# Optimization experiments

Hardware: AMD Instinct MI355X
Metric: run time of the kernel (lower is better)

Reference implementation:

```python
import jax, jax.numpy as jnp
import numpy as np

V = 32000   # vocab_size
H = 256     # num_hiddens
B = 32      # batch
T = 128     # seq_len


def setup_inputs() -> dict:
    key = jax.random.key(0)
    ks = jax.random.split(key, 10)
    s = 0.05  # keep pre-activations in a sane range
    return {
        "X": jax.random.randint(ks[0], (B, T), 0, V),
        "H0": jnp.zeros((B, H), jnp.float32),
        "Wz": (jax.random.normal(ks[1], (H, V + H)) * s).astype(jnp.float32),
        "bz": (jax.random.normal(ks[2], (H,)) * s).astype(jnp.float32),
        "Wr": (jax.random.normal(ks[3], (H, V + H)) * s).astype(jnp.float32),
        "br": (jax.random.normal(ks[4], (H,)) * s).astype(jnp.float32),
        "Wh": (jax.random.normal(ks[5], (H, V + H)) * s).astype(jnp.float32),
        "bh": (jax.random.normal(ks[6], (H,)) * s).astype(jnp.float32),
        "Wo": (jax.random.normal(ks[7], (V, H)) * s).astype(jnp.float32),
        "bo": (jax.random.normal(ks[8], (V,)) * s).astype(jnp.float32),
    }


def reference(X, H0, Wz, bz, Wr, br, Wh, bh, Wo, bo):
    # nn.Linear(cat(one_hot(x), h)) == gather of the vocab-columns + h @ Wh.T.
    # one_hot(x) @ W[:, :V].T  ==  W[:, :V].T[x]  (row gather), same math, no dense one-hot GEMM.
    vocab = Wo.shape[0]
    Wz_x, Wz_h = Wz[:, :vocab], Wz[:, vocab:]
    Wr_x, Wr_h = Wr[:, :vocab], Wr[:, vocab:]
    Wh_x, Wh_h = Wh[:, :vocab], Wh[:, vocab:]

    Xt = X.T                 # [T, B] -- matches X.T in torch forward
    gz = Wz_x.T[Xt]          # [T, B, H]
    gr = Wr_x.T[Xt]          # [T, B, H]
    gh = Wh_x.T[Xt]          # [T, B, H]

    def step(Hs, g):
        gz_t, gr_t, gh_t = g
        z = jax.nn.sigmoid(gz_t + Hs @ Wz_h.T + bz)
        r = jax.nn.sigmoid(gr_t + Hs @ Wr_h.T + br)
        h = jnp.tanh(gh_t + (r * Hs) @ Wh_h.T + bh)
        Hn = z * h + (1.0 - z) * Hs
        Y = Hn @ Wo.T + bo   # [B, V]
        return Hn, Y

    Hf, Ys = jax.lax.scan(step, H0, (gz, gr, gh))  # Ys: [T, B, V]
    # torch.cat(outputs, dim=0) stacks time-major -> [T*B, V]
    return Ys.reshape(-1, vocab), Hf
```

## Files before the change

kernel.cpp:

```cpp
#include <hip/hip_runtime.h>
#include <hip/hip_fp16.h>
#include <stdint.h>

#define VV 32000
#define HH 256
#define BB 32
#define TT 128
#define VH 32256
#define NTILE 4000

typedef _Float16 f16;
typedef _Float16 f16x2 __attribute__((ext_vector_type(2)));
typedef _Float16 f16x8 __attribute__((ext_vector_type(8)));
typedef float f32x16 __attribute__((ext_vector_type(16)));
typedef unsigned long long u64;

static __device__ __forceinline__ float dot2f(uint32_t w, uint32_t h, float acc){
  f16x2 a = __builtin_bit_cast(f16x2, w);
  f16x2 b = __builtin_bit_cast(f16x2, h);
#if __has_builtin(__builtin_amdgcn_fdot2)
  return __builtin_amdgcn_fdot2(a, b, acc, false);
#else
  acc = fmaf((float)a[0], (float)b[0], acc);
  acc = fmaf((float)a[1], (float)b[1], acc);
  return acc;
#endif
}

__global__ void k_init(int* __restrict__ ctl){
  int i = blockIdx.x*1024 + threadIdx.x;
  if (i < 4100) ctl[i] = 0;
}

__global__ void k_gather(const int* __restrict__ X,
                         const float* __restrict__ Wz, const float* __restrict__ bz,
                         const float* __restrict__ Wr, const float* __restrict__ br,
                         const float* __restrict__ Wh, const float* __restrict__ bh,
                         float* __restrict__ g_buf){
  int tb = blockIdx.x;
  int t = tb >> 5, b = tb & 31;
  int tok = X[b*TT + t];
  int o = threadIdx.x;
  g_buf[(size_t)tb*768 + o]       = Wz[(size_t)o*VH + tok] + bz[o];
  g_buf[(size_t)tb*768 + 256 + o] = Wr[(size_t)o*VH + tok] + br[o];
  g_buf[(size_t)tb*768 + 512 + o] = Wh[(size_t)o*VH + tok] + bh[o];
}

__global__ void k_pack(const float* __restrict__ Wz, const float* __restrict__ Wr,
                       const float* __restrict__ Wh, uint32_t* __restrict__ Wpack){
  int idx = blockIdx.x*256 + threadIdx.x;
  if (idx >= 512*192) return;
  int t = idx / 192, rem = idx - t*192;
  int ol = rem >> 4, p = rem & 15;
  int ko = t & 7, no = t >> 3;
  int k = ko*32 + p*2;
  const float* W; int row;
  if (ol < 8){ int o = no*8 + ol; if (o < 256){ W = Wz; row = o; } else { W = Wr; row = o - 256; } }
  else { W = Wh; row = no*4 + (ol - 8); }
  float a = W[(size_t)row*VH + VV + k];
  float c = W[(size_t)row*VH + VV + k + 1];
  f16x2 v; v[0] = (f16)a; v[1] = (f16)c;
  Wpack[idx] = __builtin_bit_cast(uint32_t, v);
}

__global__ void k_wo(const float* __restrict__ Wo, f16* __restrict__ Wof){
  int i = blockIdx.x*256 + threadIdx.x;
  const float4* s = (const float4*)Wo + (size_t)i*2;
  float4 f0 = s[0], f1 = s[1];
  f16x8 h;
  h[0]=(f16)f0.x; h[1]=(f16)f0.y; h[2]=(f16)f0.z; h[3]=(f16)f0.w;
  h[4]=(f16)f1.x; h[5]=(f16)f1.y; h[6]=(f16)f1.z; h[7]=(f16)f1.w;
  *(f16x8*)(Wof + (size_t)i*8) = h;
}

#define DECL16(P) uint32_t P##_0,P##_1,P##_2,P##_3,P##_4,P##_5,P##_6,P##_7, \
                           P##_8,P##_9,P##_10,P##_11,P##_12,P##_13,P##_14,P##_15;
#define LDQ(j,e0,e1,e2,e3) { uint4 v_ = src[j]; \
  asm("v_accvgpr_write_b32 %0, %1" : "=a"(e0) : "v"(v_.x)); \
  asm("v_accvgpr_write_b32 %0, %1" : "=a"(e1) : "v"(v_.y)); \
  asm("v_accvgpr_write_b32 %0, %1" : "=a"(e2) : "v"(v_.z)); \
  asm("v_accvgpr_write_b32 %0, %1" : "=a"(e3) : "v"(v_.w)); }
#define LDROW(r,P) LDQ(4*(r)+0,P##_0,P##_1,P##_2,P##_3)   LDQ(4*(r)+1,P##_4,P##_5,P##_6,P##_7) \
                   LDQ(4*(r)+2,P##_8,P##_9,P##_10,P##_11) LDQ(4*(r)+3,P##_12,P##_13,P##_14,P##_15)
#define RD(a_) __extension__({ uint32_t t_; \
  asm volatile("v_accvgpr_read_b32 %0, %1" : "=v"(t_) : "a"(a_)); t_; })
#define DOTP1(p) \
  a0 = dot2f(RD(w0_##p), hp[p], a0);  a1 = dot2f(RD(w1_##p), hp[p], a1); \
  a2 = dot2f(RD(w2_##p), hp[p], a2);  a3 = dot2f(RD(w3_##p), hp[p], a3); \
  a4 = dot2f(RD(w4_##p), hp[p], a4);  a5 = dot2f(RD(w5_##p), hp[p], a5); \
  a6 = dot2f(RD(w6_##p), hp[p], a6);  a7 = dot2f(RD(w7_##p), hp[p], a7);
#define DOTP2(p) \
  b0 = dot2f(RD(w8_##p),  rp[p], b0); b1 = dot2f(RD(w9_##p),  rp[p], b1); \
  b2 = dot2f(RD(w10_##p), rp[p], b2); b3 = dot2f(RD(w11_##p), rp[p], b3);
#define REDUCE(x) x += __shfl_xor(x,1); x += __shfl_xor(x,2); x += __shfl_xor(x,4);

__global__ __launch_bounds__(512)
__attribute__((amdgpu_waves_per_eu(2, 2)))
void k_main(const float* __restrict__ H0, const uint32_t* __restrict__ Wpack,
            const float* __restrict__ g_buf,
            const f16* __restrict__ Wof, const float* __restrict__ bo,
            f16* __restrict__ Hn16, float* __restrict__ Y, float* __restrict__ hf_out,
            int* __restrict__ ctl){
  __shared__ __align__(16) f16 a_lds[128*128];
  __shared__ __align__(16) f16 b_lds[256*128];
  __shared__ __align__(16) uint32_t hs16[128];
  __shared__ __align__(16) f16 rHs16[256];
  __shared__ float hs32[256];
  __shared__ float z_s[256];
  __shared__ int sh_role, sh_tile;
  const int tid = threadIdx.x;
  if (tid == 0) sh_role = atomicAdd(&ctl[4096], 1);
  __syncthreads();
  const int role = sh_role;

  if (role < BB){
    const int b = role;
    const int ko = tid & 7, no = tid >> 3;

    DECL16(w0) DECL16(w1) DECL16(w2)  DECL16(w3)  DECL16(w4)  DECL16(w5)
    DECL16(w6) DECL16(w7) DECL16(w8)  DECL16(w9)  DECL16(w10) DECL16(w11)
    {
      const uint4* src = (const uint4*)(Wpack + (size_t)tid*192);
      LDROW(0,w0) LDROW(1,w1) LDROW(2,w2)   LDROW(3,w3)  LDROW(4,w4)  LDROW(5,w5)
      LDROW(6,w6) LDROW(7,w7) LDROW(8,w8)   LDROW(9,w9)  LDROW(10,w10) LDROW(11,w11)
    }

    if (tid < 256) hs32[tid] = H0[b*HH + tid];
    __syncthreads();
    if (tid < 128){
      f16x2 v; v[0] = (f16)hs32[2*tid]; v[1] = (f16)hs32[2*tid+1];
      hs16[tid] = __builtin_bit_cast(uint32_t, v);
    }
    __syncthreads();

    const int gi1 = no*8 + ko;
    const int gi2 = 512 + no*4 + (ko & 3);
    float g1 = g_buf[(size_t)b*768 + gi1];
    float g2 = g_buf[(size_t)b*768 + gi2];
    float g1n = 0.f, g2n = 0.f;

    for (int t = 0; t < TT; t++){
      if (t < TT-1){
        const float* gn = g_buf + (size_t)((t+1)*BB + b)*768;
        g1n = gn[gi1];
        g2n = gn[gi2];
      }

      uint32_t hp[16];
      {
        const uint2* hsp = (const uint2*)hs16;
        #pragma unroll
        for (int j=0;j<8;j++){ uint2 v = hsp[ko*8 + j]; hp[2*j] = v.x; hp[2*j+1] = v.y; }
      }
      float a0=0.f,a1=0.f,a2=0.f,a3=0.f,a4=0.f,a5=0.f,a6=0.f,a7=0.f;
      DOTP1(0)  DOTP1(1)  DOTP1(2)  DOTP1(3)  DOTP1(4)  DOTP1(5)  DOTP1(6)  DOTP1(7)
      DOTP1(8)  DOTP1(9)  DOTP1(10) DOTP1(11) DOTP1(12) DOTP1(13) DOTP1(14) DOTP1(15)
      REDUCE(a0) REDUCE(a1) REDUCE(a2) REDUCE(a3) REDUCE(a4) REDUCE(a5) REDUCE(a6) REDUCE(a7)
      {
        float sel = a0;
        sel = (ko==1)?a1:sel; sel = (ko==2)?a2:sel; sel = (ko==3)?a3:sel;
        sel = (ko==4)?a4:sel; sel = (ko==5)?a5:sel; sel = (ko==6)?a6:sel; sel = (ko==7)?a7:sel;
        float pre = sel + g1;
        float s = 1.f / (1.f + __expf(-pre));
        int o = no*8 + ko;
        if (no < 32){
          z_s[o] = s;
        } else {
          int op = o - 256;
          rHs16[op] = (f16)(s * hs32[op]);
        }
      }
      __syncthreads();

      uint32_t rp[16];
      {
        const uint2* rpp = (const uint2*)rHs16;
        #pragma unroll
        for (int j=0;j<8;j++){ uint2 v = rpp[ko*8 + j]; rp[2*j] = v.x; rp[2*j+1] = v.y; }
      }
      float b0=0.f,b1=0.f,b2=0.f,b3=0.f;
      DOTP2(0)  DOTP2(1)  DOTP2(2)  DOTP2(3)  DOTP2(4)  DOTP2(5)  DOTP2(6)  DOTP2(7)
      DOTP2(8)  DOTP2(9)  DOTP2(10) DOTP2(11) DOTP2(12) DOTP2(13) DOTP2(14) DOTP2(15)
      REDUCE(b0) REDUCE(b1) REDUCE(b2) REDUCE(b3)
      if (ko < 4){
        float sel = b0;
        sel = (ko==1)?b1:sel; sel = (ko==2)?b2:sel; sel = (ko==3)?b3:sel;
        int o = no*4 + ko;
        float pre = sel + g2;
        float ax = fabsf(pre);
        float e = __expf(2.f*ax);
        float th = 1.f - 2.f/(e + 1.f);
        th = copysignf(th, pre);
        float z = z_s[o];
        float hn = z*th + (1.f - z)*hs32[o];
        hs32[o] = hn;
        ((f16*)hs16)[o] = (f16)hn;
        if (t == TT-1) hf_out[b*HH + o] = hn;
      }
      g1 = g1n; g2 = g2n;
      __syncthreads();
      if (tid < 64){
        u64 v = ((const u64*)hs16)[tid];
        __hip_atomic_store((u64*)(Hn16 + ((size_t)(t*BB + b) << 8)) + tid, v,
                           __ATOMIC_RELAXED, __HIP_MEMORY_SCOPE_AGENT);
      }
      if (tid == 0){
        asm volatile("s_waitcnt vmcnt(0)" ::: "memory");
        __hip_atomic_fetch_add(&ctl[t*32], 1, __ATOMIC_RELAXED, __HIP_MEMORY_SCOPE_AGENT);
      }
    }
  }

  {
    const int lane = tid & 63, wid = tid >> 6;
    const int wm = wid & 1, wn = wid >> 1;
    const int arow = tid >> 2, aseg = tid & 3;
    const int brow = tid >> 1, bseg = tid & 1;
    int fenced_t = -1;
    for (;;){
      if (tid == 0) sh_tile = atomicAdd(&ctl[4097], 1);
      __syncthreads();
      const int tile = sh_tile;
      if (tile >= NTILE) break;
      const int mg = tile / 125;
      const int ng = tile - mg*125;
      const int m0 = mg*128, n0 = ng*256;
      const int t_need = mg*4 + 3;
      if (tid == 0 && t_need > fenced_t){
        while (__hip_atomic_load(&ctl[t_need*32], __ATOMIC_RELAXED, __HIP_MEMORY_SCOPE_AGENT) < BB)
          __builtin_amdgcn_s_sleep(16);
        __threadfence();
        fenced_t = t_need;
      }
      __syncthreads();

      f32x16 acc[2][2];
      {
        f32x16 z = {0.f};
        acc[0][0]=z; acc[0][1]=z; acc[1][0]=z; acc[1][1]=z;
      }

      #pragma unroll 1
      for (int kt=0; kt<2; kt++){
        {
          const uint4* asrc = (const uint4*)(Hn16 + (size_t)(m0+arow)*HH + kt*128 + aseg*32);
          #pragma unroll
          for (int j=0;j<4;j++){
            uint4 v = asrc[j];
            int byte = arow*256 + ((aseg*64 + j*16) ^ ((arow&15)<<4));
            *(uint4*)((char*)a_lds + byte) = v;
          }
          const uint4* bsrc = (const uint4*)(Wof + (size_t)(n0+brow)*HH + kt*128 + bseg*64);
          #pragma unroll
          for (int j=0;j<8;j++){
            uint4 v = bsrc[j];
            int byte = brow*256 + ((bseg*128 + j*16) ^ ((brow&15)<<4));
            *(uint4*)((char*)b_lds + byte) = v;
          }
        }
        __syncthreads();
        #pragma unroll
        for (int kk=0; kk<8; kk++){
          const int kbyte = kk*32 + (lane>>5)*16;
          f16x8 af[2], bf[2];
          #pragma unroll
          for (int mi=0;mi<2;mi++){
            int row = wm*64 + mi*32 + (lane&31);
            int byte = row*256 + (kbyte ^ ((row&15)<<4));
            af[mi] = *(const f16x8*)((const char*)a_lds + byte);
          }
          #pragma unroll
          for (int nj=0;nj<2;nj++){
            int nl = wn*64 + nj*32 + (lane&31);
            int byte = nl*256 + (kbyte ^ ((nl&15)<<4));
            bf[nj] = *(const f16x8*)((const char*)b_lds + byte);
          }
          #pragma unroll
          for (int mi=0;mi<2;mi++)
            #pragma unroll
            for (int nj=0;nj<2;nj++)
              acc[mi][nj] = __builtin_amdgcn_mfma_f32_32x32x16_f16(af[mi], bf[nj], acc[mi][nj], 0, 0, 0);
        }
        __syncthreads();
      }
      #pragma unroll
      for (int nj=0;nj<2;nj++){
        const int col = n0 + wn*64 + nj*32 + (lane & 31);
        const float bov = bo[col];
        #pragma unroll
        for (int mi=0;mi<2;mi++){
          const int rbase = m0 + wm*64 + mi*32 + 4*(lane>>5);
          #pragma unroll
          for (int r=0;r<16;r++){
            int row = rbase + (r&3) + 8*(r>>2);
            Y[(size_t)row*VV + col] = acc[mi][nj][r] + bov;
          }
        }
      }
    }
  }
}

extern "C" void kernel_launch(void* const* d_in, const int* in_sizes, int n_in,
                              void* d_out, int out_size, void* d_ws, size_t ws_size,
                              hipStream_t stream){
  const int*   X  = (const int*)d_in[0];
  const float* H0 = (const float*)d_in[1];
  const float* Wz = (const float*)d_in[2];
  const float* bz = (const float*)d_in[3];
  const float* Wr = (const float*)d_in[4];
  const float* br = (const float*)d_in[5];
  const float* Wh = (const float*)d_in[6];
  const float* bh = (const float*)d_in[7];
  const float* Wo = (const float*)d_in[8];
  const float* bo = (const float*)d_in[9];
  float* out = (float*)d_out;

  char* ws = (char*)d_ws;
  int*      ctl   = (int*)ws;
  uint32_t* Wpack = (uint32_t*)(ws + 16512);
  f16*      Hn16  = (f16*)(ws + 409728);
  f16*      Wof   = (f16*)(ws + 2506880);
  float*    g_buf = (float*)(ws + 18890880);

  k_init<<<5, 1024, 0, stream>>>(ctl);
  k_gather<<<4096, 256, 0, stream>>>(X, Wz, bz, Wr, br, Wh, bh, g_buf);
  k_pack<<<384, 256, 0, stream>>>(Wz, Wr, Wh, Wpack);
  k_wo<<<4000, 256, 0, stream>>>(Wo, Wof);
  k_main<<<256, 512, 0, stream>>>(H0, Wpack, g_buf, Wof, bo, Hn16, out, out + 131072000LL, ctl);
}
```

Baseline: 533.9 us.

## Fuse prep kernels into one launch and publish hidden states every four steps

Merges the init, gather, pack and Wo-conversion kernels into a single block-indexed prep kernel, removing three launches and the gaps between them. In the recurrent producer, each step's fp16 hidden state now goes to a shared-memory staging ring. The ring is flushed to global memory, and the progress counter bumped, only once every four timesteps. This cuts per-step global stores, waits and atomics on the serial critical path, but delays when the output GEMM tiles can start on fresh rows. It also relies on consumers only waiting on the counters for every fourth timestep.

```diff
diff --git a/kernel.cpp b/kernel.cpp
--- a/kernel.cpp
+++ b/kernel.cpp
@@ -27,50 +27,48 @@
 #endif
 }
 
-__global__ void k_init(int* __restrict__ ctl){
-  int i = blockIdx.x*1024 + threadIdx.x;
-  if (i < 4100) ctl[i] = 0;
-}
-
-__global__ void k_gather(const int* __restrict__ X,
-                         const float* __restrict__ Wz, const float* __restrict__ bz,
-                         const float* __restrict__ Wr, const float* __restrict__ br,
-                         const float* __restrict__ Wh, const float* __restrict__ bh,
-                         float* __restrict__ g_buf){
-  int tb = blockIdx.x;
-  int t = tb >> 5, b = tb & 31;
-  int tok = X[b*TT + t];
-  int o = threadIdx.x;
-  g_buf[(size_t)tb*768 + o]       = Wz[(size_t)o*VH + tok] + bz[o];
-  g_buf[(size_t)tb*768 + 256 + o] = Wr[(size_t)o*VH + tok] + br[o];
-  g_buf[(size_t)tb*768 + 512 + o] = Wh[(size_t)o*VH + tok] + bh[o];
-}
-
-__global__ void k_pack(const float* __restrict__ Wz, const float* __restrict__ Wr,
-                       const float* __restrict__ Wh, uint32_t* __restrict__ Wpack){
-  int idx = blockIdx.x*256 + threadIdx.x;
-  if (idx >= 512*192) return;
-  int t = idx / 192, rem = idx - t*192;
-  int ol = rem >> 4, p = rem & 15;
-  int ko = t & 7, no = t >> 3;
-  int k = ko*32 + p*2;
-  const float* W; int row;
-  if (ol < 8){ int o = no*8 + ol; if (o < 256){ W = Wz; row = o; } else { W = Wr; row = o - 256; } }
-  else { W = Wh; row = no*4 + (ol - 8); }
-  float a = W[(size_t)row*VH + VV + k];
-  float c = W[(size_t)row*VH + VV + k + 1];
-  f16x2 v; v[0] = (f16)a; v[1] = (f16)c;
-  Wpack[idx] = __builtin_bit_cast(uint32_t, v);
-}
-
-__global__ void k_wo(const float* __restrict__ Wo, f16* __restrict__ Wof){
-  int i = blockIdx.x*256 + threadIdx.x;
-  const float4* s = (const float4*)Wo + (size_t)i*2;
-  float4 f0 = s[0], f1 = s[1];
-  f16x8 h;
-  h[0]=(f16)f0.x; h[1]=(f16)f0.y; h[2]=(f16)f0.z; h[3]=(f16)f0.w;
-  h[4]=(f16)f1.x; h[5]=(f16)f1.y; h[6]=(f16)f1.z; h[7]=(f16)f1.w;
-  *(f16x8*)(Wof + (size_t)i*8) = h;
+__global__ void k_prep(const int* __restrict__ X,
+                       const float* __restrict__ Wz, const float* __restrict__ bz,
+                       const float* __restrict__ Wr, const float* __restrict__ br,
+                       const float* __restrict__ Wh, const float* __restrict__ bh,
+                       const float* __restrict__ Wo,
+                       float* __restrict__ g_buf, uint32_t* __restrict__ Wpack,
+                       f16* __restrict__ Wof, int* __restrict__ ctl){
+  const int bid = blockIdx.x;
+  const int tidx = threadIdx.x;
+  if (bid < 4096){
+    int t = bid >> 5, b = bid & 31;
+    int tok = X[b*TT + t];
+    int o = tidx;
+    g_buf[(size_t)bid*768 + o]       = Wz[(size_t)o*VH + tok] + bz[o];
+    g_buf[(size_t)bid*768 + 256 + o] = Wr[(size_t)o*VH + tok] + br[o];
+    g_buf[(size_t)bid*768 + 512 + o] = Wh[(size_t)o*VH + tok] + bh[o];
+  } else if (bid < 4480){
+    int idx = (bid - 4096)*256 + tidx;
+    if (idx < 512*192){
+      int t = idx / 192, rem = idx - t*192;
+      int ol = rem >> 4, p = rem & 15;
+      int ko = t & 7, no = t >> 3;
+      int k = ko*32 + p*2;
+      const float* W; int row;
+      if (ol < 8){ int o = no*8 + ol; if (o < 256){ W = Wz; row = o; } else { W = Wr; row = o - 256; } }
+      else { W = Wh; row = no*4 + (ol - 8); }
+      float a = W[(size_t)row*VH + VV + k];
+      float c = W[(size_t)row*VH + VV + k + 1];
+      f16x2 v; v[0] = (f16)a; v[1] = (f16)c;
+      Wpack[idx] = __builtin_bit_cast(uint32_t, v);
+    }
+  } else if (bid < 8480){
+    int i = (bid - 4480)*256 + tidx;
+    const float4* s = (const float4*)Wo + (size_t)i*2;
+    float4 f0 = s[0], f1 = s[1];
+    f16x8 h;
+    h[0]=(f16)f0.x; h[1]=(f16)f0.y; h[2]=(f16)f0.z; h[3]=(f16)f0.w;
+    h[4]=(f16)f1.x; h[5]=(f16)f1.y; h[6]=(f16)f1.z; h[7]=(f16)f1.w;
+    *(f16x8*)(Wof + (size_t)i*8) = h;
+  } else {
+    for (int i = tidx; i < 4100; i += 256) ctl[i] = 0;
+  }
 }
 
 #define DECL16(P) uint32_t P##_0,P##_1,P##_2,P##_3,P##_4,P##_5,P##_6,P##_7, \
@@ -105,6 +103,7 @@
   __shared__ __align__(16) f16 b_lds[256*128];
   __shared__ __align__(16) uint32_t hs16[128];
   __shared__ __align__(16) f16 rHs16[256];
+  __shared__ __align__(16) u64 hstage[256];
   __shared__ float hs32[256];
   __shared__ float z_s[256];
   __shared__ int sh_role, sh_tile;
@@ -195,18 +194,22 @@
         float hn = z*th + (1.f - z)*hs32[o];
         hs32[o] = hn;
         ((f16*)hs16)[o] = (f16)hn;
+        ((f16*)hstage)[(t&3)*256 + o] = (f16)hn;
         if (t == TT-1) hf_out[b*HH + o] = hn;
       }
       g1 = g1n; g2 = g2n;
       __syncthreads();
-      if (tid < 64){
-        u64 v = ((const u64*)hs16)[tid];
-        __hip_atomic_store((u64*)(Hn16 + ((size_t)(t*BB + b) << 8)) + tid, v,
-                           __ATOMIC_RELAXED, __HIP_MEMORY_SCOPE_AGENT);
-      }
-      if (tid == 0){
-        asm volatile("s_waitcnt vmcnt(0)" ::: "memory");
-        __hip_atomic_fetch_add(&ctl[t*32], 1, __ATOMIC_RELAXED, __HIP_MEMORY_SCOPE_AGENT);
+      if ((t & 3) == 3){
+        if (tid < 256){
+          int s = tid >> 6, lane = tid & 63;
+          int tr = t - 3 + s;
+          u64 v = hstage[tid];
+          __hip_atomic_store(((u64*)Hn16) + (((size_t)(tr*BB + b)) << 6) + lane, v,
+                             __ATOMIC_RELAXED, __HIP_MEMORY_SCOPE_AGENT);
+        }
+        __syncthreads();
+        if (tid == 0)
+          __hip_atomic_fetch_add(&ctl[t*32], 1, __ATOMIC_RELAXED, __HIP_MEMORY_SCOPE_AGENT);
       }
     }
   }
@@ -323,9 +326,6 @@
   f16*      Wof   = (f16*)(ws + 2506880);
   float*    g_buf = (float*)(ws + 18890880);
 
-  k_init<<<5, 1024, 0, stream>>>(ctl);
-  k_gather<<<4096, 256, 0, stream>>>(X, Wz, bz, Wr, br, Wh, bh, g_buf);
-  k_pack<<<384, 256, 0, stream>>>(Wz, Wr, Wh, Wpack);
-  k_wo<<<4000, 256, 0, stream>>>(Wo, Wof);
+  k_prep<<<8481, 256, 0, stream>>>(X, Wz, bz, Wr, br, Wh, bh, Wo, g_buf, Wpack, Wof, ctl);
   k_main<<<256, 512, 0, stream>>>(H0, Wpack, g_buf, Wof, bo, Hn16, out, out + 131072000LL, ctl);
 }
```

After: 476.0 us. 1.12x faster.
